# Performance work log

Measured on AMD Instinct MI355X. Metric: run time of the kernel, lower is better.

## Reference

```python
import jax, jax.numpy as jnp
import numpy as np

HIDDEN = 128
AUG = 2          # aug_dim
SUBSTEPS = 2     # fixed dopri5 substeps per output interval (replaces adaptive stepping)
B = 16384
T = 8


def _xavier(key, shape, gain=5.0 / 3.0):
    fan_in, fan_out = shape
    lim = gain * np.sqrt(6.0 / (fan_in + fan_out))
    return jax.random.uniform(key, shape, jnp.float32, -lim, lim)


def setup_inputs() -> dict:
    key = jax.random.key(0)
    ks = jax.random.split(key, 4)
    return {
        "r0": jax.random.normal(ks[0], (B, 2), jnp.float32),
        "t": jnp.linspace(0.0, 1.0, T, dtype=jnp.float32),
        "W1": _xavier(ks[1], (5, HIDDEN)),
        "b1": jnp.zeros((HIDDEN,), jnp.float32),
        "W2": _xavier(ks[2], (HIDDEN, HIDDEN)),
        "b2": jnp.zeros((HIDDEN,), jnp.float32),
        "W3": _xavier(ks[3], (HIDDEN, 2)),
        "b3": jnp.zeros((2,), jnp.float32),
    }


def _ode_f(t, s, W1, b1, W2, b2, W3, b3):
    # s: [B, 2+AUG]; t: scalar -> concat time feature, tiny tanh MLP
    tf = t * jnp.ones((s.shape[0], 1), s.dtype)
    inp = jnp.concatenate([s, tf], axis=-1)            # [B, 5]
    h = jnp.tanh(inp @ W1 + b1)                        # [B, 128]
    h = jnp.tanh(h @ W2 + b2)                          # [B, 128]
    v_xy = h @ W3 + b3                                 # [B, 2]
    v_a = jnp.zeros((s.shape[0], AUG), s.dtype)        # static aug dynamics
    return jnp.concatenate([v_xy, v_a], axis=-1)


def _dopri5_step(f, t, s, dt):
    # Dormand-Prince RK45 tableau, 5th-order solution advance (as torchdiffeq dopri5)
    k1 = f(t, s)
    k2 = f(t + dt * (1.0 / 5.0), s + dt * (1.0 / 5.0) * k1)
    k3 = f(t + dt * (3.0 / 10.0), s + dt * ((3.0 / 40.0) * k1 + (9.0 / 40.0) * k2))
    k4 = f(t + dt * (4.0 / 5.0),
           s + dt * ((44.0 / 45.0) * k1 - (56.0 / 15.0) * k2 + (32.0 / 9.0) * k3))
    k5 = f(t + dt * (8.0 / 9.0),
           s + dt * ((19372.0 / 6561.0) * k1 - (25360.0 / 2187.0) * k2
                     + (64448.0 / 6561.0) * k3 - (212.0 / 729.0) * k4))
    k6 = f(t + dt,
           s + dt * ((9017.0 / 3168.0) * k1 - (355.0 / 33.0) * k2
                     + (46732.0 / 5247.0) * k3 + (49.0 / 176.0) * k4
                     - (5103.0 / 18656.0) * k5))
    return s + dt * ((35.0 / 384.0) * k1 + (500.0 / 1113.0) * k3
                     + (125.0 / 192.0) * k4 - (2187.0 / 6784.0) * k5
                     + (11.0 / 84.0) * k6)


def _integrate(r0, t, W1, b1, W2, b2, W3, b3):
    s0 = jnp.concatenate([r0, jnp.zeros((r0.shape[0], AUG), r0.dtype)], axis=-1)
    f = lambda tt, ss: _ode_f(tt, ss, W1, b1, W2, b2, W3, b3)

    def interval(s, ts):
        t0, t1 = ts
        dt = (t1 - t0) / SUBSTEPS
        for j in range(SUBSTEPS):  # small fixed loop, unrolled
            s = _dopri5_step(f, t0 + j * dt, s, dt)
        return s, s

    _, ys = jax.lax.scan(interval, s0, (t[:-1], t[1:]))   # [T-1, B, 4]
    traj = jnp.concatenate([s0[None], ys], axis=0)        # [T, B, 4]
    return jnp.transpose(traj, (1, 0, 2))[..., :2]        # [B, T, 2]


def reference(r0, t, W1, b1, W2, b2, W3, b3):
    return _integrate(r0, t, W1, b1, W2, b2, W3, b3)
```

## Files before the change

### kernel.cpp

```cpp
#include <hip/hip_runtime.h>


#define HID 128
#define TT  8
#define F(a,b) ((float)((double)(a)/(double)(b)))
#define K2C 2.8853900817779268f

typedef __attribute__((ext_vector_type(8))) short bf16x8;
typedef __attribute__((ext_vector_type(4))) float f32x4;
typedef __attribute__((ext_vector_type(2))) float f32x2;

union Frag { bf16x8 v; unsigned short u[8]; unsigned int d[4]; };

__device__ __forceinline__ f32x2 bc(float s) { return f32x2{s, s}; }
__device__ __forceinline__ f32x2 pk_fma(f32x2 a, f32x2 b, f32x2 c) {
#if __has_builtin(__builtin_elementwise_fma)
  return __builtin_elementwise_fma(a, b, c);
#else
  return a * b + c;
#endif
}
__device__ __forceinline__ float exp2_fast(float x) {
#if __has_builtin(__builtin_amdgcn_exp2f)
  return __builtin_amdgcn_exp2f(x);
#else
  return __builtin_exp2f(x);
#endif
}
__device__ __forceinline__ unsigned short f2bf(float f) {
  unsigned u = __builtin_bit_cast(unsigned, f);
  u += 0x7FFFu + ((u >> 16) & 1u);
  return (unsigned short)(u >> 16);
}
__device__ __forceinline__ unsigned pack2bf(float a, float b) {
  unsigned ua = __builtin_bit_cast(unsigned, a);
  unsigned ub = __builtin_bit_cast(unsigned, b);
  ua += 0x7FFFu + ((ua >> 16) & 1u);
  ub += 0x7FFFu + ((ub >> 16) & 1u);
  return __builtin_amdgcn_perm(ub, ua, 0x07060302u);
}
__device__ __forceinline__ f32x2 tanh_pre(f32x2 u) {
  f32x2 e;
  e.x = exp2_fast(u.x);
  e.y = exp2_fast(u.y);
  f32x2 d = e + bc(1.0f);
  f32x2 r;
  r.x = __builtin_amdgcn_rcpf(d.x);
  r.y = __builtin_amdgcn_rcpf(d.y);
  return pk_fma(bc(-2.0f), r, bc(1.0f));
}

__global__ __launch_bounds__(64, 1) void node_kernel(
    const float* __restrict__ r0, const float* __restrict__ tarr,
    const float* __restrict__ W1, const float* __restrict__ b1,
    const float* __restrict__ W2, const float* __restrict__ b2,
    const float* __restrict__ W3, const float* __restrict__ b3,
    float* __restrict__ out)
{
  const int lane = (int)(threadIdx.x & 63u);
  const int quad = lane >> 4;
  const int m16  = lane & 15;
  const int s    = (int)blockIdx.x * 16 + m16;

  f32x2 w1x[16], w1y[16], w1t[16], bb1[16];
  #pragma unroll
  for (int kk = 0; kk < 4; ++kk)
    #pragma unroll
    for (int p = 0; p < 4; ++p) {
      int i = kk * 32 + quad * 8 + 2 * p;
      int idx = kk * 4 + p;
      w1x[idx] = f32x2{W1[0 * HID + i], W1[0 * HID + i + 1]} * bc(K2C);
      w1y[idx] = f32x2{W1[1 * HID + i], W1[1 * HID + i + 1]} * bc(K2C);
      w1t[idx] = f32x2{W1[4 * HID + i], W1[4 * HID + i + 1]} * bc(K2C);
      bb1[idx] = f32x2{b1[i], b1[i + 1]} * bc(K2C);
    }
  Frag W2f[8][4];
  #pragma unroll
  for (int t = 0; t < 8; ++t) {
    int o = t * 16 + m16;
    #pragma unroll
    for (int kk = 0; kk < 4; ++kk)
      #pragma unroll
      for (int j = 0; j < 8; ++j)
        W2f[t][kk].u[j] = f2bf(W2[(kk * 32 + quad * 8 + j) * HID + o] * K2C);
  }
  f32x4 b2i[8];
  f32x2 w3v[8][4];
  #pragma unroll
  for (int t = 0; t < 8; ++t)
    #pragma unroll
    for (int rr = 0; rr < 4; ++rr) {
      int o = t * 16 + quad * 4 + rr;
      b2i[t][rr] = b2[o] * K2C;
      w3v[t][rr] = f32x2{W3[o * 2 + 0], W3[o * 2 + 1]};
    }
  const f32x2 b3v = f32x2{b3[0], b3[1]};

  f32x2 S = f32x2{r0[2 * s + 0], r0[2 * s + 1]};
  if (lane < 16) *(float2*)&out[(s * TT + 0) * 2] = make_float2(S.x, S.y);

  auto feval = [&](float tt, f32x2 st) -> f32x2 {
    const f32x2 sx = bc(st.x), sy = bc(st.y), tv = bc(tt);
    unsigned hd[16];
    #pragma unroll
    for (int idx = 0; idx < 16; ++idx) {
      f32x2 a = pk_fma(sx, w1x[idx], bb1[idx]);
      a = pk_fma(sy, w1y[idx], a);
      a = pk_fma(tv, w1t[idx], a);
      f32x2 h = tanh_pre(a);
      hd[idx] = pack2bf(h.x, h.y);
    }
    f32x4 acc[8];
    #pragma unroll
    for (int t = 0; t < 8; ++t) acc[t] = b2i[t];
    #pragma unroll
    for (int kk = 0; kk < 4; ++kk) {
      Frag bv;
      bv.d[0] = hd[kk * 4 + 0]; bv.d[1] = hd[kk * 4 + 1];
      bv.d[2] = hd[kk * 4 + 2]; bv.d[3] = hd[kk * 4 + 3];
      #pragma unroll
      for (int t = 0; t < 8; ++t)
        acc[t] = __builtin_amdgcn_mfma_f32_16x16x32_bf16(W2f[t][kk].v, bv.v, acc[t], 0, 0, 0);
    }
    f32x2 vs = bc(0.f);
    #pragma unroll
    for (int t = 0; t < 8; ++t)
      #pragma unroll
      for (int p = 0; p < 2; ++p) {
        f32x2 av = f32x2{acc[t][2 * p], acc[t][2 * p + 1]};
        f32x2 h2 = tanh_pre(av);
        vs = pk_fma(bc(h2.x), w3v[t][2 * p + 0], vs);
        vs = pk_fma(bc(h2.y), w3v[t][2 * p + 1], vs);
      }
    float px = vs.x, py = vs.y;
    px += __shfl_xor(px, 16); px += __shfl_xor(px, 32);
    py += __shfl_xor(py, 16); py += __shfl_xor(py, 32);
    return f32x2{px, py} + b3v;
  };

  #pragma unroll 1
  for (int iv = 0; iv < TT - 1; ++iv) {
    float t0 = tarr[iv], t1 = tarr[iv + 1];
    float dt = (t1 - t0) * 0.5f;
    #pragma unroll 1
    for (int ss = 0; ss < 2; ++ss) {
      float tb = (ss == 0) ? t0 : (t0 + dt);
      const f32x2 dtv = bc(dt);
      f32x2 k1 = feval(tb, S);
      f32x2 k2 = feval(tb + dt * F(1,5), pk_fma(bc(dt * F(1,5)), k1, S));
      f32x2 a3 = pk_fma(bc(F(9,40)), k2, bc(F(3,40)) * k1);
      f32x2 k3 = feval(tb + dt * F(3,10), pk_fma(dtv, a3, S));
      f32x2 a4 = pk_fma(bc(F(44,45)), k1,
                 pk_fma(bc(-F(56,15)), k2, bc(F(32,9)) * k3));
      f32x2 k4 = feval(tb + dt * F(4,5), pk_fma(dtv, a4, S));
      f32x2 a5 = pk_fma(bc(F(19372,6561)), k1,
                 pk_fma(bc(-F(25360,2187)), k2,
                 pk_fma(bc(F(64448,6561)), k3, bc(-F(212,729)) * k4)));
      f32x2 k5 = feval(tb + dt * F(8,9), pk_fma(dtv, a5, S));
      f32x2 a6 = pk_fma(bc(F(9017,3168)), k1,
                 pk_fma(bc(-F(355,33)), k2,
                 pk_fma(bc(F(46732,5247)), k3,
                 pk_fma(bc(F(49,176)), k4, bc(-F(5103,18656)) * k5))));
      f32x2 k6 = feval(tb + dt, pk_fma(dtv, a6, S));
      f32x2 fin = pk_fma(bc(F(35,384)), k1,
                  pk_fma(bc(F(500,1113)), k3,
                  pk_fma(bc(F(125,192)), k4,
                  pk_fma(bc(-F(2187,6784)), k5, bc(F(11,84)) * k6))));
      S = pk_fma(dtv, fin, S);
    }
    if (lane < 16) *(float2*)&out[(s * TT + iv + 1) * 2] = make_float2(S.x, S.y);
  }
}

extern "C" void kernel_launch(void* const* d_in, const int* in_sizes, int n_in,
                              void* d_out, int out_size, void* d_ws, size_t ws_size,
                              hipStream_t stream) {
  const float* r0 = (const float*)d_in[0];
  const float* t  = (const float*)d_in[1];
  const float* W1 = (const float*)d_in[2];
  const float* b1 = (const float*)d_in[3];
  const float* W2 = (const float*)d_in[4];
  const float* b2 = (const float*)d_in[5];
  const float* W3 = (const float*)d_in[6];
  const float* b3 = (const float*)d_in[7];
  float* out = (float*)d_out;
  const int B = in_sizes[0] / 2;
  dim3 grid(B / 16), block(64);
  node_kernel<<<grid, block, 0, stream>>>(r0, t, W1, b1, W2, b2, W3, b3, out);
}
```

Measured before the change: 195.5 us.

## Split each 16-sample MLP evaluation across four waves via LDS exchange

Each block now uses four waves instead of one for the same 16 samples. Each wave computes a quarter of the hidden-1 activations and two of the eight output tiles of the 128x128 layer. Activations and partial output sums are exchanged through shared memory with two barriers per function evaluation. This cuts per-thread register use and work per wave, which allows more parallelism and shorter serial chains per sample. The cost is barrier and LDS traffic, plus four times as many threads, on a latency-bound RK loop.

```diff
diff --git a/kernel.cpp b/kernel.cpp
--- a/kernel.cpp
+++ b/kernel.cpp
@@ -50,92 +50,103 @@
   return pk_fma(bc(-2.0f), r, bc(1.0f));
 }
 
-__global__ __launch_bounds__(64, 1) void node_kernel(
+__global__ __launch_bounds__(256, 2) void node_kernel(
     const float* __restrict__ r0, const float* __restrict__ tarr,
     const float* __restrict__ W1, const float* __restrict__ b1,
     const float* __restrict__ W2, const float* __restrict__ b2,
     const float* __restrict__ W3, const float* __restrict__ b3,
     float* __restrict__ out)
 {
-  const int lane = (int)(threadIdx.x & 63u);
+  __shared__ uint4  h1L[16][16];
+  __shared__ float2 vpS[16][4];
+
+  const int tid  = (int)threadIdx.x;
+  const int lane = tid & 63;
+  const int w    = __builtin_amdgcn_readfirstlane(tid >> 6);
   const int quad = lane >> 4;
   const int m16  = lane & 15;
+  const int g    = w * 4 + quad;
   const int s    = (int)blockIdx.x * 16 + m16;
 
-  f32x2 w1x[16], w1y[16], w1t[16], bb1[16];
+  f32x2 w1x[4], w1y[4], w1t[4], bb1[4];
   #pragma unroll
-  for (int kk = 0; kk < 4; ++kk)
-    #pragma unroll
-    for (int p = 0; p < 4; ++p) {
-      int i = kk * 32 + quad * 8 + 2 * p;
-      int idx = kk * 4 + p;
-      w1x[idx] = f32x2{W1[0 * HID + i], W1[0 * HID + i + 1]} * bc(K2C);
-      w1y[idx] = f32x2{W1[1 * HID + i], W1[1 * HID + i + 1]} * bc(K2C);
-      w1t[idx] = f32x2{W1[4 * HID + i], W1[4 * HID + i + 1]} * bc(K2C);
-      bb1[idx] = f32x2{b1[i], b1[i + 1]} * bc(K2C);
-    }
-  Frag W2f[8][4];
+  for (int p = 0; p < 4; ++p) {
+    int i = g * 8 + 2 * p;
+    w1x[p] = f32x2{W1[0 * HID + i], W1[0 * HID + i + 1]} * bc(K2C);
+    w1y[p] = f32x2{W1[1 * HID + i], W1[1 * HID + i + 1]} * bc(K2C);
+    w1t[p] = f32x2{W1[4 * HID + i], W1[4 * HID + i + 1]} * bc(K2C);
+    bb1[p] = f32x2{b1[i], b1[i + 1]} * bc(K2C);
+  }
+  Frag W2f[2][4];
   #pragma unroll
-  for (int t = 0; t < 8; ++t) {
-    int o = t * 16 + m16;
+  for (int oti = 0; oti < 2; ++oti) {
+    int o = (2 * w + oti) * 16 + m16;
     #pragma unroll
     for (int kk = 0; kk < 4; ++kk)
       #pragma unroll
       for (int j = 0; j < 8; ++j)
-        W2f[t][kk].u[j] = f2bf(W2[(kk * 32 + quad * 8 + j) * HID + o] * K2C);
+        W2f[oti][kk].u[j] = f2bf(W2[(kk * 32 + quad * 8 + j) * HID + o] * K2C);
   }
-  f32x4 b2i[8];
-  f32x2 w3v[8][4];
+  f32x4 b2i[2];
+  f32x2 w3v[2][4];
   #pragma unroll
-  for (int t = 0; t < 8; ++t)
+  for (int oti = 0; oti < 2; ++oti)
     #pragma unroll
     for (int rr = 0; rr < 4; ++rr) {
-      int o = t * 16 + quad * 4 + rr;
-      b2i[t][rr] = b2[o] * K2C;
-      w3v[t][rr] = f32x2{W3[o * 2 + 0], W3[o * 2 + 1]};
+      int o = (2 * w + oti) * 16 + quad * 4 + rr;
+      b2i[oti][rr] = b2[o] * K2C;
+      w3v[oti][rr] = f32x2{W3[o * 2 + 0], W3[o * 2 + 1]};
     }
   const f32x2 b3v = f32x2{b3[0], b3[1]};
 
   f32x2 S = f32x2{r0[2 * s + 0], r0[2 * s + 1]};
-  if (lane < 16) *(float2*)&out[(s * TT + 0) * 2] = make_float2(S.x, S.y);
+  if (tid < 16) *(float2*)&out[(s * TT + 0) * 2] = make_float2(S.x, S.y);
 
   auto feval = [&](float tt, f32x2 st) -> f32x2 {
     const f32x2 sx = bc(st.x), sy = bc(st.y), tv = bc(tt);
-    unsigned hd[16];
-    #pragma unroll
-    for (int idx = 0; idx < 16; ++idx) {
-      f32x2 a = pk_fma(sx, w1x[idx], bb1[idx]);
-      a = pk_fma(sy, w1y[idx], a);
-      a = pk_fma(tv, w1t[idx], a);
-      f32x2 h = tanh_pre(a);
-      hd[idx] = pack2bf(h.x, h.y);
-    }
-    f32x4 acc[8];
-    #pragma unroll
-    for (int t = 0; t < 8; ++t) acc[t] = b2i[t];
+    {
+      unsigned pd[4];
+      #pragma unroll
+      for (int p = 0; p < 4; ++p) {
+        f32x2 a = pk_fma(sx, w1x[p], bb1[p]);
+        a = pk_fma(sy, w1y[p], a);
+        a = pk_fma(tv, w1t[p], a);
+        f32x2 h = tanh_pre(a);
+        pd[p] = pack2bf(h.x, h.y);
+      }
+      h1L[g][m16] = make_uint4(pd[0], pd[1], pd[2], pd[3]);
+    }
+    __syncthreads();
+    f32x4 acc[2];
+    acc[0] = b2i[0]; acc[1] = b2i[1];
     #pragma unroll
     for (int kk = 0; kk < 4; ++kk) {
       Frag bv;
-      bv.d[0] = hd[kk * 4 + 0]; bv.d[1] = hd[kk * 4 + 1];
-      bv.d[2] = hd[kk * 4 + 2]; bv.d[3] = hd[kk * 4 + 3];
-      #pragma unroll
-      for (int t = 0; t < 8; ++t)
-        acc[t] = __builtin_amdgcn_mfma_f32_16x16x32_bf16(W2f[t][kk].v, bv.v, acc[t], 0, 0, 0);
+      uint4 t4 = h1L[kk * 4 + quad][m16];
+      bv.d[0] = t4.x; bv.d[1] = t4.y; bv.d[2] = t4.z; bv.d[3] = t4.w;
+      acc[0] = __builtin_amdgcn_mfma_f32_16x16x32_bf16(W2f[0][kk].v, bv.v, acc[0], 0, 0, 0);
+      acc[1] = __builtin_amdgcn_mfma_f32_16x16x32_bf16(W2f[1][kk].v, bv.v, acc[1], 0, 0, 0);
     }
     f32x2 vs = bc(0.f);
     #pragma unroll
-    for (int t = 0; t < 8; ++t)
+    for (int oti = 0; oti < 2; ++oti)
       #pragma unroll
       for (int p = 0; p < 2; ++p) {
-        f32x2 av = f32x2{acc[t][2 * p], acc[t][2 * p + 1]};
+        f32x2 av = f32x2{acc[oti][2 * p], acc[oti][2 * p + 1]};
         f32x2 h2 = tanh_pre(av);
-        vs = pk_fma(bc(h2.x), w3v[t][2 * p + 0], vs);
-        vs = pk_fma(bc(h2.y), w3v[t][2 * p + 1], vs);
+        vs = pk_fma(bc(h2.x), w3v[oti][2 * p + 0], vs);
+        vs = pk_fma(bc(h2.y), w3v[oti][2 * p + 1], vs);
       }
     float px = vs.x, py = vs.y;
     px += __shfl_xor(px, 16); px += __shfl_xor(px, 32);
     py += __shfl_xor(py, 16); py += __shfl_xor(py, 32);
-    return f32x2{px, py} + b3v;
+    if (lane < 16) vpS[m16][w] = make_float2(px, py);
+    __syncthreads();
+    float4 q0 = *(const float4*)&vpS[m16][0];
+    float4 q1 = *(const float4*)&vpS[m16][2];
+    f32x2 rv = b3v + f32x2{q0.x, q0.y} + f32x2{q0.z, q0.w}
+                   + f32x2{q1.x, q1.y} + f32x2{q1.z, q1.w};
+    return rv;
   };
 
   #pragma unroll 1
@@ -168,7 +179,7 @@
                   pk_fma(bc(-F(2187,6784)), k5, bc(F(11,84)) * k6))));
       S = pk_fma(dtv, fin, S);
     }
-    if (lane < 16) *(float2*)&out[(s * TT + iv + 1) * 2] = make_float2(S.x, S.y);
+    if (tid < 16) *(float2*)&out[(s * TT + iv + 1) * 2] = make_float2(S.x, S.y);
   }
 }
 
@@ -185,6 +196,6 @@
   const float* b3 = (const float*)d_in[7];
   float* out = (float*)d_out;
   const int B = in_sizes[0] / 2;
-  dim3 grid(B / 16), block(64);
+  dim3 grid(B / 16), block(256);
   node_kernel<<<grid, block, 0, stream>>>(r0, t, W1, b1, W2, b2, W3, b3, out);
 }
```

Result: no change. 191.8 us (-1.9%).
